# Optimization experiments

Measured on AMD Instinct MI355X. Metric: run time of the kernel, lower is better.

The kernel has to match this reference:

```python
import jax, jax.numpy as jnp
import numpy as np

N_USERS = 100000
N_ITEMS = 50000
N_NODES = N_USERS + N_ITEMS
NNZ = 4000000
BATCH = 16384
DIM = 64
ALPHA = 0.1
K_LAYERS = 3


def setup_inputs() -> dict:
    key = jax.random.key(0)
    ks = jax.random.split(key, 7)
    user_emb = 0.1 * jax.random.normal(ks[0], (N_USERS, DIM), dtype=jnp.float32)
    item_emb = 0.1 * jax.random.normal(ks[1], (N_ITEMS, DIM), dtype=jnp.float32)
    edge_vals = jax.random.uniform(ks[2], (NNZ,), dtype=jnp.float32)
    row = jax.random.randint(ks[3], (NNZ,), 0, N_NODES, dtype=jnp.int32)
    col = jax.random.randint(ks[4], (NNZ,), 0, N_NODES, dtype=jnp.int32)
    users = jax.random.randint(ks[5], (BATCH,), 0, N_USERS, dtype=jnp.int32)
    items = jax.random.randint(ks[6], (BATCH,), 0, N_ITEMS, dtype=jnp.int32)
    return {"user_emb": user_emb, "item_emb": item_emb, "edge_vals": edge_vals,
            "row": row, "col": col, "users": users, "items": items}


def _propagate(user_emb, item_emb, edge_vals, row, col):
    # computer(): concat user/item embeddings, then APPNP/PPR-style propagation
    # x^{k+1} = alpha * x0 + (1-alpha) * A x^k   (A sparse COO, symmetric-normalized)
    x0 = jnp.concatenate([user_emb, item_emb], axis=0)  # [N, d]
    x = x0
    w = edge_vals[:, None]
    for _ in range(K_LAYERS):
        msg = w * x[col]  # gather: [nnz, d]
        agg = jax.ops.segment_sum(msg, row, num_segments=N_NODES)  # scatter-add spmm
        x = ALPHA * x0 + (1.0 - ALPHA) * agg
    return x[:N_USERS], x[N_USERS:]


def reference(user_emb, item_emb, edge_vals, row, col, users, items):
    all_users, all_items = _propagate(user_emb, item_emb, edge_vals, row, col)
    u = all_users[users]   # [B, d]
    i = all_items[items]   # [B, d]
    gamma = jnp.sum(u * i, axis=1)  # [B]
    return gamma
```

## Files before the change

kernel.cpp:

```cpp
#include <hip/hip_runtime.h>

#define N_USERS 100000
#define N_ITEMS 50000
#define N_NODES 150000
#define NNZ_EDGES 4000000
#define BATCH_SZ 16384
#define DIM 64
#define ALPHA 0.1f
#define BETA 0.9f

#define BKT_SHIFT 10
#define BKT_ROWS  (1 << BKT_SHIFT)
#define NBKT      ((N_NODES + BKT_ROWS - 1) >> BKT_SHIFT)
#define BKT_PAD   16
#define BIN_CHUNK 4096
#define N_BIN_BLOCKS ((NNZ_EDGES + BIN_CHUNK - 1) / BIN_CHUNK)
#define SEG_MAX   1024
#define EDGES_PER_THREAD 30

__device__ __forceinline__ unsigned short gtn_f2bf(float f) {
    unsigned int u = __float_as_uint(f);
    u = u + 0x7FFFu + ((u >> 16) & 1u);
    return (unsigned short)(u >> 16);
}
__device__ __forceinline__ unsigned int gtn_pack_bf16x2(float lo, float hi) {
    return ((unsigned int)gtn_f2bf(lo)) | (((unsigned int)gtn_f2bf(hi)) << 16);
}

__global__ void gtn_cvt_kernel(const float* __restrict__ xu,
                               const float* __restrict__ xi,
                               unsigned short* __restrict__ x0b) {
    const int total4 = N_NODES * DIM / 4;
    const int boundary4 = N_USERS * DIM / 4;
    for (int i4 = blockIdx.x * blockDim.x + threadIdx.x; i4 < total4;
         i4 += gridDim.x * blockDim.x) {
        const float4 v = (i4 < boundary4)
            ? ((const float4*)xu)[i4]
            : ((const float4*)xi)[i4 - boundary4];
        ushort4 o;
        o.x = gtn_f2bf(v.x);
        o.y = gtn_f2bf(v.y);
        o.z = gtn_f2bf(v.z);
        o.w = gtn_f2bf(v.w);
        ((ushort4*)x0b)[i4] = o;
    }
}

__global__ void gtn_bin_sort_kernel(const int* __restrict__ row,
                                    const int* __restrict__ col,
                                    const float* __restrict__ w,
                                    int2* __restrict__ binned,
                                    int2* __restrict__ blkSeg,
                                    int* __restrict__ bucketTotal) {
    __shared__ int hist[NBKT];
    __shared__ int scanb[512];
    __shared__ int cursor[NBKT];
    __shared__ int2 stage[BIN_CHUNK];
    const int blk = blockIdx.x;
    const int t = threadIdx.x;
    const int chunkStart = blk * BIN_CHUNK;
    const int chunkN = min(BIN_CHUNK, NNZ_EDGES - chunkStart);

    for (int b = t; b < NBKT; b += 512) hist[b] = 0;
    __syncthreads();

    int rloc[BIN_CHUNK / 512];
#pragma unroll
    for (int k = 0; k < BIN_CHUNK / 512; ++k) {
        const int i = t + k * 512;
        int r = -1;
        if (i < chunkN) {
            r = row[chunkStart + i];
            atomicAdd(&hist[r >> BKT_SHIFT], 1);
        }
        rloc[k] = r;
    }
    __syncthreads();

    const int hv = (t < NBKT) ? hist[t] : 0;
    scanb[t] = hv;
    __syncthreads();
    for (int off = 1; off < 512; off <<= 1) {
        const int tv = (t >= off) ? scanb[t - off] : 0;
        __syncthreads();
        scanb[t] += tv;
        __syncthreads();
    }
    if (t < NBKT) {
        const int exc = scanb[t] - hv;
        cursor[t] = exc;
        blkSeg[(size_t)t * N_BIN_BLOCKS + blk] = make_int2(exc, hv);
        if (hv) atomicAdd(&bucketTotal[t * BKT_PAD], hv);
    }
    __syncthreads();

#pragma unroll
    for (int k = 0; k < BIN_CHUNK / 512; ++k) {
        const int i = t + k * 512;
        if (i < chunkN) {
            const int r = rloc[k];
            const int b = r >> BKT_SHIFT;
            const int pos = atomicAdd(&cursor[b], 1);
            stage[pos] = make_int2(col[chunkStart + i] | ((r & (BKT_ROWS - 1)) << 18),
                                   __float_as_int(w[chunkStart + i]));
        }
    }
    __syncthreads();

    int2* dst = binned + (size_t)chunkStart;
#pragma unroll
    for (int k = 0; k < BIN_CHUNK / 512; ++k) {
        const int i = t + k * 512;
        if (i < chunkN) dst[i] = stage[i];
    }
}

__global__ void gtn_bktbase_kernel(const int* __restrict__ bucketTotal,
                                   int* __restrict__ bktBase) {
    __shared__ int s[512];
    const int t = threadIdx.x;
    const int v = (t < NBKT) ? bucketTotal[t * BKT_PAD] : 0;
    s[t] = v;
    __syncthreads();
    for (int off = 1; off < 512; off <<= 1) {
        const int tv = (t >= off) ? s[t - off] : 0;
        __syncthreads();
        s[t] += tv;
        __syncthreads();
    }
    if (t < NBKT) bktBase[t] = s[t] - v;
}

__global__ void gtn_bucket_csr_kernel(const int2* __restrict__ binned,
                                      const int2* __restrict__ blkSeg,
                                      const int* __restrict__ bktBase,
                                      int* __restrict__ rowPtr,
                                      int* __restrict__ cnt,
                                      int2* __restrict__ colw) {
    __shared__ int incl[SEG_MAX];
    __shared__ int segIdx[SEG_MAX];
    __shared__ int hist[BKT_ROWS];
    __shared__ int scan[BKT_ROWS];
    __shared__ int cursor[BKT_ROWS];
    const int b = blockIdx.x;
    const int t = threadIdx.x;

    int2 seg = make_int2(0, 0);
    if (t < N_BIN_BLOCKS) seg = blkSeg[(size_t)b * N_BIN_BLOCKS + t];
    segIdx[t] = t * BIN_CHUNK + seg.x;
    incl[t] = seg.y;
    hist[t] = 0;
    __syncthreads();
    for (int off = 1; off < SEG_MAX; off <<= 1) {
        const int tv = (t >= off) ? incl[t - off] : 0;
        __syncthreads();
        incl[t] += tv;
        __syncthreads();
    }
    const int n = incl[SEG_MAX - 1];

    int2 e[EDGES_PER_THREAD];
#pragma unroll
    for (int k = 0; k < EDGES_PER_THREAD; ++k) {
        const int i = t + k * 1024;
        if (i < n) {
            int s = 0;
#pragma unroll
            for (int st = 512; st > 0; st >>= 1) {
                const int c = s + st;
                if (c <= SEG_MAX && incl[c - 1] <= i) s = c;
            }
            const int base = s ? incl[s - 1] : 0;
            e[k] = binned[(size_t)segIdx[s] + (i - base)];
            atomicAdd(&hist[((unsigned)e[k].x) >> 18], 1);
        }
    }
    __syncthreads();

    const int v = hist[t];
    scan[t] = v;
    __syncthreads();
    for (int off = 1; off < BKT_ROWS; off <<= 1) {
        const int tv = (t >= off) ? scan[t - off] : 0;
        __syncthreads();
        scan[t] += tv;
        __syncthreads();
    }
    const int g = (b << BKT_SHIFT) + t;
    const int pos0 = bktBase[b] + scan[t] - v;
    if (g < N_NODES) { cnt[g] = v; rowPtr[g] = pos0; }
    cursor[t] = pos0;
    __syncthreads();

#pragma unroll
    for (int k = 0; k < EDGES_PER_THREAD; ++k) {
        const int i = t + k * 1024;
        if (i < n) {
            const int inrow = ((unsigned)e[k].x) >> 18;
            const int pos = atomicAdd(&cursor[inrow], 1);
            colw[pos] = make_int2(e[k].x & 0x3FFFF, e[k].y);
        }
    }
}

__device__ __forceinline__ void gtn_gather_row8(
        int node, int lane, int sub, int grp,
        const unsigned short* __restrict__ x,
        const int* __restrict__ rowPtr, const int* __restrict__ cnt,
        const int2* __restrict__ colw, float acc[8]) {
    const int start = rowPtr[node];
    const int n = cnt[node];
    for (int base = 0; base < n; base += 64) {
        const int m = min(64, n - base);
        int2 e = make_int2(0, 0);
        if (lane < m) e = colw[start + base + lane];
        const int nk = (m + 7) >> 3;
        for (int kb = 0; kb < nk; kb += 4) {
            uint4 xv[4];
            float wv[4];
#pragma unroll
            for (int k = 0; k < 4; ++k) {
                const int src = ((kb + k) << 3) + grp;
                const int c = __shfl(e.x, src, 64);
                wv[k] = __int_as_float(__shfl(e.y, src, 64));
                xv[k] = *(const uint4*)(x + ((size_t)c << 6) + (sub << 3));
            }
#pragma unroll
            for (int k = 0; k < 4; ++k) {
                acc[0] = fmaf(wv[k], __uint_as_float(xv[k].x << 16), acc[0]);
                acc[1] = fmaf(wv[k], __uint_as_float(xv[k].x & 0xFFFF0000u), acc[1]);
                acc[2] = fmaf(wv[k], __uint_as_float(xv[k].y << 16), acc[2]);
                acc[3] = fmaf(wv[k], __uint_as_float(xv[k].y & 0xFFFF0000u), acc[3]);
                acc[4] = fmaf(wv[k], __uint_as_float(xv[k].z << 16), acc[4]);
                acc[5] = fmaf(wv[k], __uint_as_float(xv[k].z & 0xFFFF0000u), acc[5]);
                acc[6] = fmaf(wv[k], __uint_as_float(xv[k].w << 16), acc[6]);
                acc[7] = fmaf(wv[k], __uint_as_float(xv[k].w & 0xFFFF0000u), acc[7]);
            }
        }
    }
}

__device__ __forceinline__ void gtn_reduce_groups8(float acc[8]) {
#pragma unroll
    for (int off = 8; off <= 32; off <<= 1) {
#pragma unroll
        for (int d = 0; d < 8; ++d) acc[d] += __shfl_xor(acc[d], off, 64);
    }
}

__global__ void gtn_layer_kernel(const unsigned short* __restrict__ x,
                                 const float* __restrict__ x0u,
                                 const float* __restrict__ x0i,
                                 const int* __restrict__ rowPtr,
                                 const int* __restrict__ cnt,
                                 const int2* __restrict__ colw,
                                 unsigned short* __restrict__ out) {
    const int lane = threadIdx.x & 63;
    const int sub = lane & 7;
    const int grp = lane >> 3;
    const int node = (blockIdx.x * blockDim.x + threadIdx.x) >> 6;
    if (node >= N_NODES) return;
    float acc[8] = {0.f, 0.f, 0.f, 0.f, 0.f, 0.f, 0.f, 0.f};
    gtn_gather_row8(node, lane, sub, grp, x, rowPtr, cnt, colw, acc);
    gtn_reduce_groups8(acc);
    if (grp == 0) {
        const float* x0p = (node < N_USERS)
            ? x0u + (size_t)node * DIM + (sub << 3)
            : x0i + (size_t)(node - N_USERS) * DIM + (sub << 3);
        const float4 a = ((const float4*)x0p)[0];
        const float4 c = ((const float4*)x0p)[1];
        uint4 o;
        o.x = gtn_pack_bf16x2(ALPHA * a.x + BETA * acc[0], ALPHA * a.y + BETA * acc[1]);
        o.y = gtn_pack_bf16x2(ALPHA * a.z + BETA * acc[2], ALPHA * a.w + BETA * acc[3]);
        o.z = gtn_pack_bf16x2(ALPHA * c.x + BETA * acc[4], ALPHA * c.y + BETA * acc[5]);
        o.w = gtn_pack_bf16x2(ALPHA * c.z + BETA * acc[6], ALPHA * c.w + BETA * acc[7]);
        *(uint4*)(out + (size_t)node * DIM + (sub << 3)) = o;
    }
}

__global__ void gtn_l3_dot_kernel(const unsigned short* __restrict__ x,
                                  const float* __restrict__ x0u,
                                  const float* __restrict__ x0i,
                                  const int* __restrict__ rowPtr,
                                  const int* __restrict__ cnt,
                                  const int2* __restrict__ colw,
                                  const int* __restrict__ users,
                                  const int* __restrict__ items,
                                  float* __restrict__ out) {
    const int lane = threadIdx.x & 63;
    const int sub = lane & 7;
    const int grp = lane >> 3;
    const int b = (blockIdx.x * blockDim.x + threadIdx.x) >> 6;
    if (b >= BATCH_SZ) return;
    const int u = users[b];
    const int it = items[b] + N_USERS;

    float au[8] = {0.f, 0.f, 0.f, 0.f, 0.f, 0.f, 0.f, 0.f};
    float ai[8] = {0.f, 0.f, 0.f, 0.f, 0.f, 0.f, 0.f, 0.f};
    gtn_gather_row8(u, lane, sub, grp, x, rowPtr, cnt, colw, au);
    gtn_reduce_groups8(au);
    gtn_gather_row8(it, lane, sub, grp, x, rowPtr, cnt, colw, ai);
    gtn_reduce_groups8(ai);

    const float* x0up = x0u + (size_t)u * DIM + (sub << 3);
    const float* x0ip = x0i + (size_t)(it - N_USERS) * DIM + (sub << 3);
    const float4 ua = ((const float4*)x0up)[0];
    const float4 ub = ((const float4*)x0up)[1];
    const float4 ia = ((const float4*)x0ip)[0];
    const float4 ib = ((const float4*)x0ip)[1];

    float p = 0.f;
    p += (ALPHA * ua.x + BETA * au[0]) * (ALPHA * ia.x + BETA * ai[0]);
    p += (ALPHA * ua.y + BETA * au[1]) * (ALPHA * ia.y + BETA * ai[1]);
    p += (ALPHA * ua.z + BETA * au[2]) * (ALPHA * ia.z + BETA * ai[2]);
    p += (ALPHA * ua.w + BETA * au[3]) * (ALPHA * ia.w + BETA * ai[3]);
    p += (ALPHA * ub.x + BETA * au[4]) * (ALPHA * ib.x + BETA * ai[4]);
    p += (ALPHA * ub.y + BETA * au[5]) * (ALPHA * ib.y + BETA * ai[5]);
    p += (ALPHA * ub.z + BETA * au[6]) * (ALPHA * ib.z + BETA * ai[6]);
    p += (ALPHA * ub.w + BETA * au[7]) * (ALPHA * ib.w + BETA * ai[7]);
    p += __shfl_xor(p, 1, 64);
    p += __shfl_xor(p, 2, 64);
    p += __shfl_xor(p, 4, 64);
    if (lane == 0) out[b] = p;
}

extern "C" void kernel_launch(void* const* d_in, const int* in_sizes, int n_in,
                              void* d_out, int out_size, void* d_ws, size_t ws_size,
                              hipStream_t stream) {
    const float* user_emb  = (const float*)d_in[0];
    const float* item_emb  = (const float*)d_in[1];
    const float* edge_vals = (const float*)d_in[2];
    const int*   row       = (const int*)d_in[3];
    const int*   col       = (const int*)d_in[4];
    const int*   users     = (const int*)d_in[5];
    const int*   items     = (const int*)d_in[6];
    float* out = (float*)d_out;

    char* p = (char*)d_ws;
    unsigned short* x0b  = (unsigned short*)p; p += (size_t)N_NODES * DIM * 2;
    unsigned short* bufA = (unsigned short*)p; p += (size_t)N_NODES * DIM * 2;
    unsigned short* bufB = (unsigned short*)p; p += (size_t)N_NODES * DIM * 2;
    int2*  colw        = (int2*)p; p += (size_t)NNZ_EDGES * sizeof(int2);
    int2*  binned      = (int2*)p; p += (size_t)NNZ_EDGES * sizeof(int2);
    int2*  blkSeg      = (int2*)p; p += (size_t)NBKT * N_BIN_BLOCKS * sizeof(int2);
    int*   bucketTotal = (int*)p;  p += (size_t)NBKT * BKT_PAD * sizeof(int);
    int*   bktBase     = (int*)p;  p += 512 * sizeof(int);
    int*   cnt         = (int*)p;  p += (size_t)N_NODES * sizeof(int);
    int*   rowPtr      = (int*)p;  p += (size_t)N_NODES * sizeof(int);

    const dim3 blk(256);

    hipMemsetAsync(bucketTotal, 0, (size_t)NBKT * BKT_PAD * sizeof(int), stream);
    gtn_bin_sort_kernel<<<dim3(N_BIN_BLOCKS), dim3(512), 0, stream>>>(
        row, col, edge_vals, binned, blkSeg, bucketTotal);
    gtn_cvt_kernel<<<dim3(2048), blk, 0, stream>>>(user_emb, item_emb, x0b);
    gtn_bktbase_kernel<<<dim3(1), dim3(512), 0, stream>>>(bucketTotal, bktBase);
    gtn_bucket_csr_kernel<<<dim3(NBKT), dim3(1024), 0, stream>>>(
        binned, blkSeg, bktBase, rowPtr, cnt, colw);

    const dim3 layerGrid((N_NODES * 64 + 255) / 256);
    gtn_layer_kernel<<<layerGrid, blk, 0, stream>>>(
        x0b, user_emb, item_emb, rowPtr, cnt, colw, bufA);
    gtn_layer_kernel<<<layerGrid, blk, 0, stream>>>(
        bufA, user_emb, item_emb, rowPtr, cnt, colw, bufB);
    const dim3 dotGrid((BATCH_SZ * 64) / 256);
    gtn_l3_dot_kernel<<<dotGrid, blk, 0, stream>>>(
        bufB, user_emb, item_emb, rowPtr, cnt, colw, users, items, out);
}
```

Measured before the change: 281.8 us.

## Map eight nodes per wavefront with 8-lane groups instead of one node per wave

The SpMM layer kernels now give each 8-lane group its own node, so a wavefront handles 8 rows and no longer needs the cross-group shuffle reduction. The dot kernel packs 4 user/item pairs per wave and does the dot product with a shuffle between the two halves of the wave. Accumulation uses packed float2 vector FMAs. With about 27 edges per row, this removes the mostly idle lanes and the reduction overhead of the old one-row-per-wave scheme. The cost is load imbalance, since every group in a wave loops up to the wave's maximum row degree.

```diff
diff --git a/kernel.cpp b/kernel.cpp
--- a/kernel.cpp
+++ b/kernel.cpp
@@ -17,6 +17,8 @@
 #define N_BIN_BLOCKS ((NNZ_EDGES + BIN_CHUNK - 1) / BIN_CHUNK)
 #define SEG_MAX   1024
 #define EDGES_PER_THREAD 30
+
+typedef float v2f __attribute__((ext_vector_type(2)));
 
 __device__ __forceinline__ unsigned short gtn_f2bf(float f) {
     unsigned int u = __float_as_uint(f);
@@ -203,49 +205,49 @@
     }
 }
 
-__device__ __forceinline__ void gtn_gather_row8(
-        int node, int lane, int sub, int grp,
+__device__ __forceinline__ void gtn_gather_grp(
+        int start, int n, int nmax, int sub, int grp,
         const unsigned short* __restrict__ x,
-        const int* __restrict__ rowPtr, const int* __restrict__ cnt,
-        const int2* __restrict__ colw, float acc[8]) {
-    const int start = rowPtr[node];
-    const int n = cnt[node];
-    for (int base = 0; base < n; base += 64) {
-        const int m = min(64, n - base);
+        const int2* __restrict__ colw, v2f acc[4]) {
+    for (int base = 0; base < nmax; base += 8) {
         int2 e = make_int2(0, 0);
-        if (lane < m) e = colw[start + base + lane];
-        const int nk = (m + 7) >> 3;
-        for (int kb = 0; kb < nk; kb += 4) {
+        if (base + sub < n) e = colw[start + base + sub];
+#pragma unroll
+        for (int k = 0; k < 8; k += 4) {
             uint4 xv[4];
             float wv[4];
 #pragma unroll
-            for (int k = 0; k < 4; ++k) {
-                const int src = ((kb + k) << 3) + grp;
-                const int c = __shfl(e.x, src, 64);
-                wv[k] = __int_as_float(__shfl(e.y, src, 64));
-                xv[k] = *(const uint4*)(x + ((size_t)c << 6) + (sub << 3));
+            for (int q = 0; q < 4; ++q) {
+                const int srcl = (grp << 3) + k + q;
+                const int c = __shfl(e.x, srcl, 64);
+                wv[q] = __int_as_float(__shfl(e.y, srcl, 64));
+                xv[q] = *(const uint4*)(x + ((size_t)c << 6) + (sub << 3));
             }
 #pragma unroll
-            for (int k = 0; k < 4; ++k) {
-                acc[0] = fmaf(wv[k], __uint_as_float(xv[k].x << 16), acc[0]);
-                acc[1] = fmaf(wv[k], __uint_as_float(xv[k].x & 0xFFFF0000u), acc[1]);
-                acc[2] = fmaf(wv[k], __uint_as_float(xv[k].y << 16), acc[2]);
-                acc[3] = fmaf(wv[k], __uint_as_float(xv[k].y & 0xFFFF0000u), acc[3]);
-                acc[4] = fmaf(wv[k], __uint_as_float(xv[k].z << 16), acc[4]);
-                acc[5] = fmaf(wv[k], __uint_as_float(xv[k].z & 0xFFFF0000u), acc[5]);
-                acc[6] = fmaf(wv[k], __uint_as_float(xv[k].w << 16), acc[6]);
-                acc[7] = fmaf(wv[k], __uint_as_float(xv[k].w & 0xFFFF0000u), acc[7]);
+            for (int q = 0; q < 4; ++q) {
+                const v2f w2 = {wv[q], wv[q]};
+                v2f p0 = {__uint_as_float(xv[q].x << 16),
+                          __uint_as_float(xv[q].x & 0xFFFF0000u)};
+                v2f p1 = {__uint_as_float(xv[q].y << 16),
+                          __uint_as_float(xv[q].y & 0xFFFF0000u)};
+                v2f p2 = {__uint_as_float(xv[q].z << 16),
+                          __uint_as_float(xv[q].z & 0xFFFF0000u)};
+                v2f p3 = {__uint_as_float(xv[q].w << 16),
+                          __uint_as_float(xv[q].w & 0xFFFF0000u)};
+                acc[0] += w2 * p0;
+                acc[1] += w2 * p1;
+                acc[2] += w2 * p2;
+                acc[3] += w2 * p3;
             }
         }
     }
 }
 
-__device__ __forceinline__ void gtn_reduce_groups8(float acc[8]) {
-#pragma unroll
-    for (int off = 8; off <= 32; off <<= 1) {
-#pragma unroll
-        for (int d = 0; d < 8; ++d) acc[d] += __shfl_xor(acc[d], off, 64);
-    }
+__device__ __forceinline__ int gtn_wave_max(int v) {
+    v = max(v, __shfl_xor(v, 8, 64));
+    v = max(v, __shfl_xor(v, 16, 64));
+    v = max(v, __shfl_xor(v, 32, 64));
+    return v;
 }
 
 __global__ void gtn_layer_kernel(const unsigned short* __restrict__ x,
@@ -258,22 +260,33 @@
     const int lane = threadIdx.x & 63;
     const int sub = lane & 7;
     const int grp = lane >> 3;
-    const int node = (blockIdx.x * blockDim.x + threadIdx.x) >> 6;
-    if (node >= N_NODES) return;
-    float acc[8] = {0.f, 0.f, 0.f, 0.f, 0.f, 0.f, 0.f, 0.f};
-    gtn_gather_row8(node, lane, sub, grp, x, rowPtr, cnt, colw, acc);
-    gtn_reduce_groups8(acc);
-    if (grp == 0) {
+    const int wid = (blockIdx.x * blockDim.x + threadIdx.x) >> 6;
+    const int node = wid * 8 + grp;
+    if (wid * 8 >= N_NODES) return;
+    const bool valid = node < N_NODES;
+    const int nv = valid ? node : 0;
+    const int start = rowPtr[nv];
+    const int n = valid ? cnt[nv] : 0;
+    const int nmax = gtn_wave_max(n);
+
+    v2f acc[4] = {{0.f, 0.f}, {0.f, 0.f}, {0.f, 0.f}, {0.f, 0.f}};
+    gtn_gather_grp(start, n, nmax, sub, grp, x, colw, acc);
+
+    if (valid) {
         const float* x0p = (node < N_USERS)
             ? x0u + (size_t)node * DIM + (sub << 3)
             : x0i + (size_t)(node - N_USERS) * DIM + (sub << 3);
         const float4 a = ((const float4*)x0p)[0];
         const float4 c = ((const float4*)x0p)[1];
         uint4 o;
-        o.x = gtn_pack_bf16x2(ALPHA * a.x + BETA * acc[0], ALPHA * a.y + BETA * acc[1]);
-        o.y = gtn_pack_bf16x2(ALPHA * a.z + BETA * acc[2], ALPHA * a.w + BETA * acc[3]);
-        o.z = gtn_pack_bf16x2(ALPHA * c.x + BETA * acc[4], ALPHA * c.y + BETA * acc[5]);
-        o.w = gtn_pack_bf16x2(ALPHA * c.z + BETA * acc[6], ALPHA * c.w + BETA * acc[7]);
+        o.x = gtn_pack_bf16x2(ALPHA * a.x + BETA * acc[0].x,
+                              ALPHA * a.y + BETA * acc[0].y);
+        o.y = gtn_pack_bf16x2(ALPHA * a.z + BETA * acc[1].x,
+                              ALPHA * a.w + BETA * acc[1].y);
+        o.z = gtn_pack_bf16x2(ALPHA * c.x + BETA * acc[2].x,
+                              ALPHA * c.y + BETA * acc[2].y);
+        o.w = gtn_pack_bf16x2(ALPHA * c.z + BETA * acc[3].x,
+                              ALPHA * c.w + BETA * acc[3].y);
         *(uint4*)(out + (size_t)node * DIM + (sub << 3)) = o;
     }
 }
@@ -290,38 +303,45 @@
     const int lane = threadIdx.x & 63;
     const int sub = lane & 7;
     const int grp = lane >> 3;
-    const int b = (blockIdx.x * blockDim.x + threadIdx.x) >> 6;
-    if (b >= BATCH_SZ) return;
-    const int u = users[b];
-    const int it = items[b] + N_USERS;
-
-    float au[8] = {0.f, 0.f, 0.f, 0.f, 0.f, 0.f, 0.f, 0.f};
-    float ai[8] = {0.f, 0.f, 0.f, 0.f, 0.f, 0.f, 0.f, 0.f};
-    gtn_gather_row8(u, lane, sub, grp, x, rowPtr, cnt, colw, au);
-    gtn_reduce_groups8(au);
-    gtn_gather_row8(it, lane, sub, grp, x, rowPtr, cnt, colw, ai);
-    gtn_reduce_groups8(ai);
-
-    const float* x0up = x0u + (size_t)u * DIM + (sub << 3);
-    const float* x0ip = x0i + (size_t)(it - N_USERS) * DIM + (sub << 3);
-    const float4 ua = ((const float4*)x0up)[0];
-    const float4 ub = ((const float4*)x0up)[1];
-    const float4 ia = ((const float4*)x0ip)[0];
-    const float4 ib = ((const float4*)x0ip)[1];
+    const int wid = (blockIdx.x * blockDim.x + threadIdx.x) >> 6;
+    const int b = wid * 4 + (grp & 3);
+    if (wid * 4 >= BATCH_SZ) return;
+    const bool valid = b < BATCH_SZ;
+    const int bv = valid ? b : 0;
+    const bool isItem = grp >= 4;
+    const int node = isItem ? items[bv] + N_USERS : users[bv];
+    const int start = rowPtr[node];
+    const int n = valid ? cnt[node] : 0;
+    const int nmax = gtn_wave_max(n);
+
+    v2f acc[4] = {{0.f, 0.f}, {0.f, 0.f}, {0.f, 0.f}, {0.f, 0.f}};
+    gtn_gather_grp(start, n, nmax, sub, grp, x, colw, acc);
+
+    const float* x0p = isItem
+        ? x0i + (size_t)(node - N_USERS) * DIM + (sub << 3)
+        : x0u + (size_t)node * DIM + (sub << 3);
+    const float4 a = ((const float4*)x0p)[0];
+    const float4 c = ((const float4*)x0p)[1];
+    float v[8];
+    v[0] = ALPHA * a.x + BETA * acc[0].x;
+    v[1] = ALPHA * a.y + BETA * acc[0].y;
+    v[2] = ALPHA * a.z + BETA * acc[1].x;
+    v[3] = ALPHA * a.w + BETA * acc[1].y;
+    v[4] = ALPHA * c.x + BETA * acc[2].x;
+    v[5] = ALPHA * c.y + BETA * acc[2].y;
+    v[6] = ALPHA * c.z + BETA * acc[3].x;
+    v[7] = ALPHA * c.w + BETA * acc[3].y;
 
     float p = 0.f;
-    p += (ALPHA * ua.x + BETA * au[0]) * (ALPHA * ia.x + BETA * ai[0]);
-    p += (ALPHA * ua.y + BETA * au[1]) * (ALPHA * ia.y + BETA * ai[1]);
-    p += (ALPHA * ua.z + BETA * au[2]) * (ALPHA * ia.z + BETA * ai[2]);
-    p += (ALPHA * ua.w + BETA * au[3]) * (ALPHA * ia.w + BETA * ai[3]);
-    p += (ALPHA * ub.x + BETA * au[4]) * (ALPHA * ib.x + BETA * ai[4]);
-    p += (ALPHA * ub.y + BETA * au[5]) * (ALPHA * ib.y + BETA * ai[5]);
-    p += (ALPHA * ub.z + BETA * au[6]) * (ALPHA * ib.z + BETA * ai[6]);
-    p += (ALPHA * ub.w + BETA * au[7]) * (ALPHA * ib.w + BETA * ai[7]);
+#pragma unroll
+    for (int d = 0; d < 8; ++d) {
+        const float other = __shfl_xor(v[d], 32, 64);
+        p = fmaf(v[d], other, p);
+    }
     p += __shfl_xor(p, 1, 64);
     p += __shfl_xor(p, 2, 64);
     p += __shfl_xor(p, 4, 64);
-    if (lane == 0) out[b] = p;
+    if (valid && !isItem && sub == 0) out[b] = p;
 }
 
 extern "C" void kernel_launch(void* const* d_in, const int* in_sizes, int n_in,
@@ -358,12 +378,12 @@
     gtn_bucket_csr_kernel<<<dim3(NBKT), dim3(1024), 0, stream>>>(
         binned, blkSeg, bktBase, rowPtr, cnt, colw);
 
-    const dim3 layerGrid((N_NODES * 64 + 255) / 256);
+    const dim3 layerGrid((N_NODES / 8 + 3) / 4);
     gtn_layer_kernel<<<layerGrid, blk, 0, stream>>>(
         x0b, user_emb, item_emb, rowPtr, cnt, colw, bufA);
     gtn_layer_kernel<<<layerGrid, blk, 0, stream>>>(
         bufA, user_emb, item_emb, rowPtr, cnt, colw, bufB);
-    const dim3 dotGrid((BATCH_SZ * 64) / 256);
+    const dim3 dotGrid((BATCH_SZ / 4 + 3) / 4);
     gtn_l3_dot_kernel<<<dotGrid, blk, 0, stream>>>(
         bufB, user_emb, item_emb, rowPtr, cnt, colw, users, items, out);
 }
```

After: 283.7 us. About the same (+0.7%).
